# Optimization experiments

Measured on AMD Instinct MI355X. Metric: run time of the kernel, lower is better.

The kernel has to match this reference:

```python
import jax, jax.numpy as jnp
import numpy as np
from jax import lax

NUM_CLASSES = 80
CONF = 0.05
IOU_T = 0.5
K_PER_CLASS = 100   # max_detections_per_class
MAX_DET = 100       # max_detections
BOX_VAR = np.array([0.1, 0.1, 0.2, 0.2], dtype=np.float32)


def make_anchors(H, W):
    """AnchorBox.get_anchors: [x, y, w, h] anchors for strides 8..128."""
    ratios = [0.5, 1.0, 2.0]
    scales = [2.0 ** 0, 2.0 ** (1.0 / 3.0), 2.0 ** (2.0 / 3.0)]
    strides = [8, 16, 32, 64, 128]
    areas = [32.0 ** 2, 64.0 ** 2, 128.0 ** 2, 256.0 ** 2, 512.0 ** 2]
    out = []
    for stride, area in zip(strides, areas):
        fh = int(np.ceil(H / stride)); fw = int(np.ceil(W / stride))
        dims = []
        for r in ratios:
            ah = np.sqrt(area / r); aw = area / ah
            for s in scales:
                dims.append([aw * s, ah * s])
        dims = np.array(dims, dtype=np.float32)              # [9,2]
        rx = (np.arange(fw, dtype=np.float32) + 0.5) * stride
        ry = (np.arange(fh, dtype=np.float32) + 0.5) * stride
        cx, cy = np.meshgrid(rx, ry)                         # [fh,fw]
        centers = np.stack([cx, cy], axis=-1)                # [fh,fw,2]
        centers = np.tile(centers[:, :, None, :], (1, 1, 9, 1))
        d = np.tile(dims[None, None, :, :], (fh, fw, 1, 1))
        out.append(np.concatenate([centers, d], axis=-1).reshape(-1, 4))
    return np.concatenate(out, axis=0).astype(np.float32)   # [N,4]


def _iou_matrix(boxes):
    # boxes: [K,4] corner format (x1,y1,x2,y2)
    lt = jnp.maximum(boxes[:, None, :2], boxes[None, :, :2])
    rb = jnp.minimum(boxes[:, None, 2:], boxes[None, :, 2:])
    inter = jnp.prod(jnp.clip(rb - lt, 0.0), axis=-1)
    area = jnp.prod(boxes[:, 2:] - boxes[:, :2], axis=-1)
    union = area[:, None] + area[None, :] - inter
    return inter / jnp.maximum(union, 1e-8)


def _decode(predictions, anchors):
    box_pred = predictions[..., :4] * jnp.asarray(BOX_VAR)
    xy = box_pred[..., :2] * anchors[:, 2:] + anchors[:, :2]
    wh = jnp.exp(box_pred[..., 2:]) * anchors[:, 2:]
    boxes = jnp.concatenate([xy - wh / 2.0, xy + wh / 2.0], axis=-1)  # [B,N,4] corners
    cls = jax.nn.sigmoid(predictions[..., 4:])                        # [B,N,C]
    return boxes, cls


def _nms_image(boxes, cls_scores):
    # boxes [N,4], cls_scores [N,C]
    rng = jnp.arange(K_PER_CLASS)

    def per_class(scores):  # [N]
        top_s, idx = lax.top_k(scores, K_PER_CLASS)
        cb = boxes[idx]                                      # [K,4]
        iou = lax.stop_gradient(_iou_matrix(cb))
        keep0 = top_s > CONF
        def body(i, keep):
            sup = keep[i] & (iou[i] > IOU_T) & (rng > i)
            return keep & (~sup)
        keep = lax.fori_loop(0, K_PER_CLASS, body, keep0)
        return cb, jnp.where(keep, top_s, -1.0)

    cboxes, cscores = jax.vmap(per_class)(cls_scores.T)      # [C,K,4], [C,K]
    cids = jnp.broadcast_to(jnp.arange(NUM_CLASSES, dtype=jnp.float32)[:, None],
                            (NUM_CLASSES, K_PER_CLASS))
    flat_s = cscores.reshape(-1)
    flat_b = cboxes.reshape(-1, 4)
    flat_c = cids.reshape(-1)
    fs, fi = lax.top_k(flat_s, MAX_DET)
    fb = flat_b[fi]
    fc = flat_c[fi]
    mask = fs > 0.0
    valid = jnp.sum(mask).astype(jnp.int32)
    return (jnp.where(mask[:, None], fb, 0.0),
            jnp.where(mask, fs, 0.0),
            jnp.where(mask, fc, 0.0),
            valid)


def setup_inputs() -> dict:
    key = jax.random.key(0)
    k1, k2 = jax.random.split(key)
    images = jax.random.normal(k1, (8, 512, 512, 3), dtype=jnp.float32)
    predictions = jax.random.normal(k2, (8, 49104, 84), dtype=jnp.float32)
    return {"images": images, "predictions": predictions}


def reference(images, predictions):
    H, W = images.shape[1], images.shape[2]
    anchors = jnp.asarray(make_anchors(H, W))                # [49104,4]
    boxes, cls = _decode(predictions, anchors)
    nmsed_boxes, nmsed_scores, nmsed_classes, valid = jax.vmap(_nms_image)(boxes, cls)
    return nmsed_boxes, nmsed_scores, nmsed_classes, valid
```

## Files before the change

### kernel.cpp

```cpp
#include <hip/hip_runtime.h>
#include <math.h>
#include <stdint.h>

#define NANCH 49104
#define NCLS 80
#define KSEL 100
#define NFLAT (NCLS * KSEL)
#define PREDC 84
#define NB 8
#define ECAP 128
#define CAP 3072
#define BATF4 (NANCH * (PREDC / 4))
#define BPB 128
#define LCAP 32
#define FASTN 512
#define RMAX 8
#define CNTP 16
#define THRL 2.5f

struct DimsTable { float d[5][9][2]; };
struct KT { uint32_t key; int tie; };

__device__ __forceinline__ uint32_t f2key(float f) {
    uint32_t u = __float_as_uint(f);
    return u ^ (uint32_t((int32_t)u >> 31) | 0x80000000u);
}
__device__ __forceinline__ float key2f(uint32_t k) {
    uint32_t u = (k & 0x80000000u) ? (k ^ 0x80000000u) : ~k;
    return __uint_as_float(u);
}
__device__ __forceinline__ float sigm(float x) { return 1.0f / (1.0f + expf(-x)); }

__device__ __forceinline__ void decode_box(const float4 pv, int n,
                                           const DimsTable& dt, float box[4]) {
    int lev, base, fw, stride;
    if (n < 36864)      { lev = 0; base = 0;     fw = 64; stride = 8;   }
    else if (n < 46080) { lev = 1; base = 36864; fw = 32; stride = 16;  }
    else if (n < 48384) { lev = 2; base = 46080; fw = 16; stride = 32;  }
    else if (n < 48960) { lev = 3; base = 48384; fw = 8;  stride = 64;  }
    else                { lev = 4; base = 48960; fw = 4;  stride = 128; }
    int i = n - base;
    int k = i % 9;
    int cell = i / 9;
    int xq = cell % fw, yq = cell / fw;
    float cx = ((float)xq + 0.5f) * (float)stride;
    float cy = ((float)yq + 0.5f) * (float)stride;
    float aw = dt.d[lev][k][0];
    float ah = dt.d[lev][k][1];
    float tx = __fmul_rn(pv.x, 0.1f);
    float ty = __fmul_rn(pv.y, 0.1f);
    float tw = __fmul_rn(pv.z, 0.2f);
    float th = __fmul_rn(pv.w, 0.2f);
    float px = __fadd_rn(__fmul_rn(tx, aw), cx);
    float py = __fadd_rn(__fmul_rn(ty, ah), cy);
    float pw = __fmul_rn(expf(tw), aw);
    float ph = __fmul_rn(expf(th), ah);
    float hw = __fmul_rn(pw, 0.5f);
    float hh = __fmul_rn(ph, 0.5f);
    box[0] = __fsub_rn(px, hw);
    box[1] = __fsub_rn(py, hh);
    box[2] = __fadd_rn(px, hw);
    box[3] = __fadd_rn(py, hh);
}

struct alignas(16) SelSh {
    int hist[4][2048];
    int suffix[256];
    uint32_t candKey[KSEL];
    int candIdx[KSEL];
    uint32_t eIdx[ECAP];
    uint32_t sKey[KSEL];
    int sIdx[KSEL];
    int cntG, cntE, krem, newkrem, digit, flast, rmin;
    uint32_t prefix, thrKey;
};

template <typename G>
__device__ int block_select(G get, int N, int K, SelSh& sh) {
    const int tid = threadIdx.x;
    const int wid = tid >> 6;
    int Ksel = (N < K) ? N : K;
    if (Ksel <= 0) return 0;

    if (N <= K) {
        if (tid < N) { KT e = get(tid); sh.candKey[tid] = e.key; sh.candIdx[tid] = e.tie; }
        __syncthreads();
        if (tid < N) {
            uint32_t mk = sh.candKey[tid]; int mi = sh.candIdx[tid];
            int rank = 0;
            for (int j = 0; j < N; ++j) {
                uint32_t kj = sh.candKey[j]; int ij = sh.candIdx[j];
                rank += (kj > mk) || (kj == mk && ij < mi);
            }
            sh.sKey[rank] = mk; sh.sIdx[rank] = mi;
        }
        __syncthreads();
        return Ksel;
    }

    if (tid == 0) { sh.krem = K; sh.prefix = 0; }
    for (int pass = 0; pass < 3; ++pass) {
        const int bins   = (pass == 2) ? 1024 : 2048;
        const int dshift = (pass == 0) ? 21 : (pass == 1 ? 10 : 0);
        const int fshift = (pass == 1) ? 21 : 10;
        const int dmask  = bins - 1;
        const bool multi = (pass == 0);
        if (multi) { for (int j = tid; j < 4 * 2048; j += 256) ((int*)sh.hist)[j] = 0; }
        else       { for (int j = tid; j < bins; j += 256) sh.hist[0][j] = 0; }
        __syncthreads();
        const uint32_t pref = sh.prefix;
        for (int i = tid; i < N; i += 256) {
            uint32_t key = get(i).key;
            if (pass == 0) {
                atomicAdd(&sh.hist[wid][(key >> dshift) & dmask], 1);
            } else if ((key >> fshift) == pref) {
                atomicAdd(&sh.hist[0][(key >> dshift) & dmask], 1);
            }
        }
        __syncthreads();
        if (multi) {
            for (int j = tid; j < bins; j += 256)
                sh.hist[0][j] += sh.hist[1][j] + sh.hist[2][j] + sh.hist[3][j];
            __syncthreads();
        }
        const int cpb = bins / 256;
        const int base = tid * cpb;
        int lsum = 0;
        for (int j = 0; j < cpb; ++j) lsum += sh.hist[0][base + j];
        sh.suffix[tid] = lsum;
        __syncthreads();
        for (int off = 1; off < 256; off <<= 1) {
            int v = (tid + off < 256) ? sh.suffix[tid + off] : 0;
            __syncthreads();
            sh.suffix[tid] += v;
            __syncthreads();
        }
        {
            int cum = sh.suffix[tid] - lsum;
            const int krem = sh.krem;
            for (int j = cpb - 1; j >= 0; --j) {
                int cnt = sh.hist[0][base + j];
                if (cnt > 0 && cum < krem && cum + cnt >= krem) {
                    sh.digit = base + j;
                    sh.newkrem = krem - cum;
                }
                cum += cnt;
            }
        }
        __syncthreads();
        if (tid == 0) {
            sh.krem = sh.newkrem;
            if (pass == 0)      sh.prefix = (uint32_t)sh.digit;
            else if (pass == 1) sh.prefix = (sh.prefix << 11) | (uint32_t)sh.digit;
            else                sh.thrKey = (sh.prefix << 10) | (uint32_t)sh.digit;
        }
        __syncthreads();
    }

    if (tid == 0) { sh.cntG = 0; sh.cntE = 0; }
    __syncthreads();
    const uint32_t thr = sh.thrKey;
    for (int i = tid; i < N; i += 256) {
        KT e = get(i);
        if (e.key > thr) {
            int g = atomicAdd(&sh.cntG, 1);
            sh.candKey[g] = e.key; sh.candIdx[g] = e.tie;
        } else if (e.key == thr) {
            int idx = atomicAdd(&sh.cntE, 1);
            if (idx < ECAP) sh.eIdx[idx] = (uint32_t)e.tie;
        }
    }
    __syncthreads();
    const int need = sh.krem;
    const int nG = K - need;
    if (sh.cntE <= ECAP) {
        const int ce = sh.cntE;
        if (tid < ce) {
            uint32_t my = sh.eIdx[tid];
            int rank = 0;
            for (int j = 0; j < ce; ++j) rank += (sh.eIdx[j] < my);
            if (rank < need) { sh.candKey[nG + rank] = thr; sh.candIdx[nG + rank] = (int)my; }
        }
    } else {
        if (tid == 0) sh.flast = -1;
        __syncthreads();
        for (int t = 0; t < need; ++t) {
            if (tid == 0) sh.rmin = 0x7FFFFFFF;
            __syncthreads();
            const int fl = sh.flast;
            int lmin = 0x7FFFFFFF;
            for (int i = tid; i < N; i += 256) {
                KT e = get(i);
                if (e.key == thr && e.tie > fl) lmin = min(lmin, e.tie);
            }
            atomicMin(&sh.rmin, lmin);
            __syncthreads();
            if (tid == 0) { sh.candKey[nG + t] = thr; sh.candIdx[nG + t] = sh.rmin; sh.flast = sh.rmin; }
            __syncthreads();
        }
    }
    __syncthreads();
    if (tid < K) {
        uint32_t mk = sh.candKey[tid]; int mi = sh.candIdx[tid];
        int rank = 0;
        for (int j = 0; j < K; ++j) {
            uint32_t kj = sh.candKey[j]; int ij = sh.candIdx[j];
            rank += (kj > mk) || (kj == mk && ij < mi);
        }
        sh.sKey[rank] = mk; sh.sIdx[rank] = mi;
    }
    __syncthreads();
    return Ksel;
}

__global__ __launch_bounds__(256) void init_k(int* __restrict__ cnt) {
    for (int x = threadIdx.x; x < (NB * NCLS + NB) * CNTP; x += 256) cnt[x] = 0;
}

__device__ __forceinline__ void procf4(float4 p, int v, int b,
                                       int* lcnt, uint2 (*buck)[LCAP],
                                       int* cnt, uint2* cand) {
    uint32_t q = (uint32_t)v / 21u;
    uint32_t j = (uint32_t)v - q * 21u;
    if (j == 0u) return;
    bool c0 = p.x > THRL, c1 = p.y > THRL, c2 = p.z > THRL, c3 = p.w > THRL;
    if (!(c0 | c1 | c2 | c3)) return;
    uint32_t row = q - (uint32_t)b * (uint32_t)NANCH;
    int cbase = ((int)j - 1) * 4;
    float vv[4] = {p.x, p.y, p.z, p.w};
    bool pp[4] = {c0, c1, c2, c3};
#pragma unroll
    for (int k = 0; k < 4; ++k) {
        if (pp[k]) {
            int c = cbase + k;
            uint32_t key = f2key(sigm(vv[k]));
            int slot = atomicAdd(&lcnt[c], 1);
            if (slot < LCAP) {
                buck[c][slot] = make_uint2(key, row);
            } else {
                int bc = b * NCLS + c;
                int gs = atomicAdd(&cnt[bc * CNTP], 1);
                if (gs < CAP) cand[(size_t)bc * CAP + gs] = make_uint2(key, row);
            }
        }
    }
}

__global__ __launch_bounds__(256) void cand_scan(const float4* __restrict__ predv,
                                                 uint2* __restrict__ cand,
                                                 int* __restrict__ cnt) {
    __shared__ uint2 buck[NCLS][LCAP];
    __shared__ int lcnt[NCLS];
    __shared__ int gbase[NCLS];

    const int tid = threadIdx.x;
    const int b = blockIdx.x / BPB;
    const int part = blockIdx.x - b * BPB;
    const int CH = (BATF4 + BPB - 1) / BPB;

    for (int j = tid; j < NCLS; j += 256) lcnt[j] = 0;
    __syncthreads();

    int s = b * BATF4 + part * CH;
    int e = b * BATF4 + BATF4;
    if (s + CH < e) e = s + CH;

    int v = s + tid;
    for (; v + 7 * 256 < e; v += 8 * 256) {
        float4 a0 = predv[v];
        float4 a1 = predv[v + 1 * 256];
        float4 a2 = predv[v + 2 * 256];
        float4 a3 = predv[v + 3 * 256];
        float4 a4 = predv[v + 4 * 256];
        float4 a5 = predv[v + 5 * 256];
        float4 a6 = predv[v + 6 * 256];
        float4 a7 = predv[v + 7 * 256];
        procf4(a0, v,           b, lcnt, buck, cnt, cand);
        procf4(a1, v + 1 * 256, b, lcnt, buck, cnt, cand);
        procf4(a2, v + 2 * 256, b, lcnt, buck, cnt, cand);
        procf4(a3, v + 3 * 256, b, lcnt, buck, cnt, cand);
        procf4(a4, v + 4 * 256, b, lcnt, buck, cnt, cand);
        procf4(a5, v + 5 * 256, b, lcnt, buck, cnt, cand);
        procf4(a6, v + 6 * 256, b, lcnt, buck, cnt, cand);
        procf4(a7, v + 7 * 256, b, lcnt, buck, cnt, cand);
    }
    for (; v < e; v += 256)
        procf4(predv[v], v, b, lcnt, buck, cnt, cand);
    __syncthreads();

    if (tid < NCLS) {
        int lc = lcnt[tid];
        if (lc > LCAP) lc = LCAP;
        gbase[tid] = (lc > 0) ? atomicAdd(&cnt[(b * NCLS + tid) * CNTP], lc) : 0;
    }
    __syncthreads();

    for (int x = tid; x < NCLS * LCAP; x += 256) {
        int c = x >> 5;
        int k = x & (LCAP - 1);
        int lc = lcnt[c];
        if (lc > LCAP) lc = LCAP;
        if (k < lc) {
            int gs = gbase[c] + k;
            if (gs < CAP)
                cand[(size_t)(b * NCLS + c) * CAP + gs] = buck[c][k];
        }
    }
}

__global__ __launch_bounds__(256) void nms_sel(const float* __restrict__ pred,
                                               const uint2* __restrict__ cand,
                                               const int* __restrict__ cnt,
                                               float* __restrict__ cls_boxes,
                                               uint32_t* __restrict__ posKey,
                                               uint32_t* __restrict__ posFlat,
                                               int* __restrict__ posCnt,
                                               DimsTable dt) {
    __shared__ SelSh sh;
    __shared__ uint16_t prank[4][FASTN];
    __shared__ float sbox[KSEL][4];
    __shared__ float sarea[KSEL];
    __shared__ int sconf[KSEL];
    __shared__ uint32_t sup[KSEL][4];
    __shared__ uint32_t keepm[4];
    __shared__ int baseSh;
    const int c = blockIdx.x;
    const int b = blockIdx.y;
    const int tid = threadIdx.x;
    const int bc = b * NCLS + c;
    const int n = cnt[bc * CNTP];

    if (n >= KSEL && n <= FASTN) {
        unsigned long long* list64 = (unsigned long long*)sh.hist;
        const uint2* src = cand + (size_t)bc * CAP;
        for (int x = tid; x < n; x += 256) {
            uint2 p = src[x];
            list64[x] = ((unsigned long long)p.x << 32) |
                        (unsigned long long)(~p.y);
        }
        __syncthreads();
        const int wid = tid >> 6;
        const int lane = tid & 63;
        unsigned long long cl[RMAX];
        int pr[RMAX];
#pragma unroll
        for (int r = 0; r < RMAX; ++r) {
            int i = r * 64 + lane;
            cl[r] = (i < n) ? list64[i] : 0xFFFFFFFFFFFFFFFFull;
            pr[r] = 0;
        }
        const int js = (wid * n) >> 2;
        const int je = ((wid + 1) * n) >> 2;
        int j = js;
        for (; j + 3 < je; j += 4) {
            unsigned long long o0 = list64[j];
            unsigned long long o1 = list64[j + 1];
            unsigned long long o2 = list64[j + 2];
            unsigned long long o3 = list64[j + 3];
#pragma unroll
            for (int r = 0; r < RMAX; ++r)
                pr[r] += (o0 > cl[r]) + (o1 > cl[r]) + (o2 > cl[r]) + (o3 > cl[r]);
        }
        for (; j < je; ++j) {
            unsigned long long o = list64[j];
#pragma unroll
            for (int r = 0; r < RMAX; ++r) pr[r] += (o > cl[r]);
        }
#pragma unroll
        for (int r = 0; r < RMAX; ++r) {
            int i = r * 64 + lane;
            if (i < n) prank[wid][i] = (uint16_t)pr[r];
        }
        __syncthreads();
        for (int i = tid; i < n; i += 256) {
            int rank = (int)prank[0][i] + (int)prank[1][i]
                     + (int)prank[2][i] + (int)prank[3][i];
            if (rank < KSEL) {
                unsigned long long e = list64[i];
                sh.sKey[rank] = (uint32_t)(e >> 32);
                sh.sIdx[rank] = (int)(~(uint32_t)e);
            }
        }
        __syncthreads();
    } else {
        const float* src = pred + (size_t)b * NANCH * PREDC + 4 + c;
        auto g = [src](int i) { KT e; e.key = f2key(sigm(src[(size_t)i * PREDC])); e.tie = i; return e; };
        block_select(g, NANCH, KSEL, sh);
    }

    for (int x = tid; x < KSEL * 4; x += 256) ((uint32_t*)sup)[x] = 0;
    if (tid < KSEL) {
        int ni = sh.sIdx[tid];
        float4 pv = reinterpret_cast<const float4*>(pred)[((size_t)b * NANCH + ni) * (PREDC / 4)];
        float bx[4]; decode_box(pv, ni, dt, bx);
        sbox[tid][0] = bx[0]; sbox[tid][1] = bx[1];
        sbox[tid][2] = bx[2]; sbox[tid][3] = bx[3];
        sarea[tid] = __fmul_rn(__fsub_rn(bx[2], bx[0]), __fsub_rn(bx[3], bx[1]));
        sconf[tid] = (key2f(sh.sKey[tid]) > 0.05f) ? 1 : 0;
    }
    __syncthreads();

    for (int pidx = tid; pidx < KSEL * KSEL; pidx += 256) {
        int i = pidx / KSEL;
        int jj = pidx - i * KSEL;
        if (jj > i && sconf[i] && sconf[jj]) {
            float x1 = fmaxf(sbox[i][0], sbox[jj][0]);
            float y1 = fmaxf(sbox[i][1], sbox[jj][1]);
            float x2 = fminf(sbox[i][2], sbox[jj][2]);
            float y2 = fminf(sbox[i][3], sbox[jj][3]);
            float iw = fmaxf(__fsub_rn(x2, x1), 0.0f);
            float ih = fmaxf(__fsub_rn(y2, y1), 0.0f);
            float inter = __fmul_rn(iw, ih);
            float uni = __fsub_rn(__fadd_rn(sarea[i], sarea[jj]), inter);
            if (__fdiv_rn(inter, fmaxf(uni, 1e-8f)) > 0.5f)
                atomicOr(&sup[i][jj >> 5], 1u << (jj & 31));
        }
    }
    __syncthreads();

    if (tid == 0) {
        uint32_t k0 = 0, k1 = 0, k2 = 0, k3 = 0;
        for (int i = 0; i < KSEL; ++i)
            if (sconf[i]) { if (i < 32) k0 |= 1u << i; else if (i < 64) k1 |= 1u << (i - 32);
                            else if (i < 96) k2 |= 1u << (i - 64); else k3 |= 1u << (i - 96); }
        for (int i = 0; i < KSEL; ++i) {
            uint32_t w = (i < 32) ? k0 : (i < 64) ? k1 : (i < 96) ? k2 : k3;
            if ((w >> (i & 31)) & 1u) {
                k0 &= ~sup[i][0]; k1 &= ~sup[i][1]; k2 &= ~sup[i][2]; k3 &= ~sup[i][3];
            }
        }
        keepm[0] = k0; keepm[1] = k1; keepm[2] = k2; keepm[3] = k3;
        baseSh = atomicAdd(&posCnt[b * CNTP],
                           __popc(k0) + __popc(k1) + __popc(k2) + __popc(k3));
    }
    __syncthreads();

    if (tid < KSEL) {
        reinterpret_cast<float4*>(cls_boxes)[(size_t)b * NFLAT + c * KSEL + tid] =
            make_float4(sbox[tid][0], sbox[tid][1], sbox[tid][2], sbox[tid][3]);
        int w = tid >> 5, bit = tid & 31;
        if ((keepm[w] >> bit) & 1u) {
            int off = __popc(keepm[w] & ((bit == 0) ? 0u : ((1u << bit) - 1u)));
            for (int ww = 0; ww < w; ++ww) off += __popc(keepm[ww]);
            posKey[(size_t)b * NFLAT + baseSh + off] = sh.sKey[tid];
            posFlat[(size_t)b * NFLAT + baseSh + off] = (uint32_t)(c * KSEL + tid);
        }
    }
}

__global__ __launch_bounds__(256) void final_sel(const float* __restrict__ cls_boxes,
                                                 const uint32_t* __restrict__ posKey,
                                                 const uint32_t* __restrict__ posFlat,
                                                 const int* __restrict__ posCnt,
                                                 float* __restrict__ out) {
    __shared__ SelSh sh;
    const int b = blockIdx.x;
    const int tid = threadIdx.x;
    int m = posCnt[b * CNTP];
    if (m > NFLAT) m = NFLAT;
    const uint32_t* pk = posKey + (size_t)b * NFLAT;
    const uint32_t* pf = posFlat + (size_t)b * NFLAT;
    auto g = [pk, pf](int i) { KT e; e.key = pk[i]; e.tie = (int)pf[i]; return e; };
    int K = block_select(g, m, KSEL, sh);
    if (tid < KSEL) {
        float4 ob = make_float4(0.f, 0.f, 0.f, 0.f);
        float sv = 0.f, cv = 0.f;
        if (tid < K) {
            sv = key2f(sh.sKey[tid]);
            int flat = sh.sIdx[tid];
            ob = reinterpret_cast<const float4*>(cls_boxes)[(size_t)b * NFLAT + flat];
            cv = (float)(flat / KSEL);
        }
        reinterpret_cast<float4*>(out)[(size_t)b * KSEL + tid] = ob;
        out[NB * KSEL * 4 + b * KSEL + tid] = sv;
        out[NB * KSEL * 5 + b * KSEL + tid] = cv;
    }
    if (tid == 0) out[NB * KSEL * 6 + b] = (float)K;
}

extern "C" void kernel_launch(void* const* d_in, const int* in_sizes, int n_in,
                              void* d_out, int out_size, void* d_ws, size_t ws_size,
                              hipStream_t stream) {
    const float* pred = (const float*)d_in[1];
    float* out = (float*)d_out;

    DimsTable dt;
    const double areasd[5] = {1024.0, 4096.0, 16384.0, 65536.0, 262144.0};
    const double ratios[3] = {0.5, 1.0, 2.0};
    const double scales[3] = {1.0, pow(2.0, 1.0 / 3.0), pow(2.0, 2.0 / 3.0)};
    for (int l = 0; l < 5; ++l)
        for (int ri = 0; ri < 3; ++ri) {
            double ah = sqrt(areasd[l] / ratios[ri]);
            double aw = areasd[l] / ah;
            for (int si = 0; si < 3; ++si) {
                dt.d[l][ri * 3 + si][0] = (float)(aw * scales[si]);
                dt.d[l][ri * 3 + si][1] = (float)(ah * scales[si]);
            }
        }

    char* wsb = (char*)d_ws;
    int* cnt = (int*)wsb;
    int* posCnt = cnt + NB * NCLS * CNTP;
    uint2* cand = (uint2*)(wsb + 64 * 1024);
    float* cls_boxes = (float*)((char*)cand + (size_t)NB * NCLS * CAP * 8);
    uint32_t* posKey = (uint32_t*)(cls_boxes + (size_t)NB * NFLAT * 4);
    uint32_t* posFlat = posKey + (size_t)NB * NFLAT;

    init_k<<<1, 256, 0, stream>>>(cnt);

    cand_scan<<<NB * BPB, 256, 0, stream>>>(reinterpret_cast<const float4*>(pred),
                                            cand, cnt);

    dim3 gb(NCLS, NB);
    nms_sel<<<gb, 256, 0, stream>>>(pred, cand, cnt, cls_boxes, posKey, posFlat,
                                    posCnt, dt);

    final_sel<<<NB, 256, 0, stream>>>(cls_boxes, posKey, posFlat, posCnt, out);
}
```

Before: 126.4 us.

## Replace global atomic candidate append with per-block slots and prefix-sum compaction

Candidate collection moves from per-class global atomic counters into fixed per-block slots (PCAP each), plus a small overflow buffer. Consumers now compact these slots with a block prefix sum, and the per-class kept lists are also written to fixed slots and compacted in final_sel. BPB is doubled, nms_sel uses a single-copy histogram to cut shared memory, and the greedy NMS keep-mask loop becomes a wavefront ballot/shuffle. This is meant to remove global atomic contention and give deterministic ordering, at the cost of extra prefix scans and a serial compaction copy in final_sel.

```diff
diff --git a/kernel.cpp b/kernel.cpp
--- a/kernel.cpp
+++ b/kernel.cpp
@@ -9,17 +9,18 @@
 #define PREDC 84
 #define NB 8
 #define ECAP 128
-#define CAP 3072
 #define BATF4 (NANCH * (PREDC / 4))
-#define BPB 128
-#define LCAP 32
+#define BPB 256
+#define PCAP 16
+#define LCAP 16
+#define OCAP 64
 #define FASTN 512
 #define RMAX 8
-#define CNTP 16
 #define THRL 2.5f
 
 struct DimsTable { float d[5][9][2]; };
 struct KT { uint32_t key; int tie; };
+typedef unsigned long long u64;
 
 __device__ __forceinline__ uint32_t f2key(float f) {
     uint32_t u = __float_as_uint(f);
@@ -63,8 +64,9 @@
     box[3] = __fadd_rn(py, hh);
 }
 
-struct alignas(16) SelSh {
-    int hist[4][2048];
+template <int NC>
+struct alignas(16) SelShT {
+    int hist[NC][2048];
     int suffix[256];
     uint32_t candKey[KSEL];
     int candIdx[KSEL];
@@ -75,8 +77,8 @@
     uint32_t prefix, thrKey;
 };
 
-template <typename G>
-__device__ int block_select(G get, int N, int K, SelSh& sh) {
+template <int NC, typename G>
+__device__ int block_select(G get, int N, int K, SelShT<NC>& sh) {
     const int tid = threadIdx.x;
     const int wid = tid >> 6;
     int Ksel = (N < K) ? N : K;
@@ -104,23 +106,25 @@
         const int dshift = (pass == 0) ? 21 : (pass == 1 ? 10 : 0);
         const int fshift = (pass == 1) ? 21 : 10;
         const int dmask  = bins - 1;
-        const bool multi = (pass == 0);
-        if (multi) { for (int j = tid; j < 4 * 2048; j += 256) ((int*)sh.hist)[j] = 0; }
-        else       { for (int j = tid; j < bins; j += 256) sh.hist[0][j] = 0; }
+        if (pass == 0) { for (int j = tid; j < NC * 2048; j += 256) ((int*)sh.hist)[j] = 0; }
+        else           { for (int j = tid; j < bins; j += 256) sh.hist[0][j] = 0; }
         __syncthreads();
         const uint32_t pref = sh.prefix;
         for (int i = tid; i < N; i += 256) {
             uint32_t key = get(i).key;
             if (pass == 0) {
-                atomicAdd(&sh.hist[wid][(key >> dshift) & dmask], 1);
+                atomicAdd(&sh.hist[(NC > 1) ? wid : 0][(key >> dshift) & dmask], 1);
             } else if ((key >> fshift) == pref) {
                 atomicAdd(&sh.hist[0][(key >> dshift) & dmask], 1);
             }
         }
         __syncthreads();
-        if (multi) {
-            for (int j = tid; j < bins; j += 256)
-                sh.hist[0][j] += sh.hist[1][j] + sh.hist[2][j] + sh.hist[3][j];
+        if (NC > 1 && pass == 0) {
+            for (int j = tid; j < bins; j += 256) {
+                int s = sh.hist[0][j];
+                for (int cc = 1; cc < NC; ++cc) s += sh.hist[cc][j];
+                sh.hist[0][j] = s;
+            }
             __syncthreads();
         }
         const int cpb = bins / 256;
@@ -213,13 +217,13 @@
     return Ksel;
 }
 
-__global__ __launch_bounds__(256) void init_k(int* __restrict__ cnt) {
-    for (int x = threadIdx.x; x < (NB * NCLS + NB) * CNTP; x += 256) cnt[x] = 0;
+__global__ __launch_bounds__(256) void init_k(int* __restrict__ oflowCnt) {
+    for (int x = threadIdx.x; x < NB * NCLS; x += 256) oflowCnt[x] = 0;
 }
 
 __device__ __forceinline__ void procf4(float4 p, int v, int b,
                                        int* lcnt, uint2 (*buck)[LCAP],
-                                       int* cnt, uint2* cand) {
+                                       int* oflowCnt, uint2* oflow) {
     uint32_t q = (uint32_t)v / 21u;
     uint32_t j = (uint32_t)v - q * 21u;
     if (j == 0u) return;
@@ -239,19 +243,20 @@
                 buck[c][slot] = make_uint2(key, row);
             } else {
                 int bc = b * NCLS + c;
-                int gs = atomicAdd(&cnt[bc * CNTP], 1);
-                if (gs < CAP) cand[(size_t)bc * CAP + gs] = make_uint2(key, row);
+                int gs = atomicAdd(&oflowCnt[bc], 1);
+                if (gs < OCAP) oflow[(size_t)bc * OCAP + gs] = make_uint2(key, row);
             }
         }
     }
 }
 
 __global__ __launch_bounds__(256) void cand_scan(const float4* __restrict__ predv,
-                                                 uint2* __restrict__ cand,
-                                                 int* __restrict__ cnt) {
+                                                 uint2* __restrict__ cand2,
+                                                 int* __restrict__ cnt2,
+                                                 int* __restrict__ oflowCnt,
+                                                 uint2* __restrict__ oflow) {
     __shared__ uint2 buck[NCLS][LCAP];
     __shared__ int lcnt[NCLS];
-    __shared__ int gbase[NCLS];
 
     const int tid = threadIdx.x;
     const int b = blockIdx.x / BPB;
@@ -275,73 +280,85 @@
         float4 a5 = predv[v + 5 * 256];
         float4 a6 = predv[v + 6 * 256];
         float4 a7 = predv[v + 7 * 256];
-        procf4(a0, v,           b, lcnt, buck, cnt, cand);
-        procf4(a1, v + 1 * 256, b, lcnt, buck, cnt, cand);
-        procf4(a2, v + 2 * 256, b, lcnt, buck, cnt, cand);
-        procf4(a3, v + 3 * 256, b, lcnt, buck, cnt, cand);
-        procf4(a4, v + 4 * 256, b, lcnt, buck, cnt, cand);
-        procf4(a5, v + 5 * 256, b, lcnt, buck, cnt, cand);
-        procf4(a6, v + 6 * 256, b, lcnt, buck, cnt, cand);
-        procf4(a7, v + 7 * 256, b, lcnt, buck, cnt, cand);
+        procf4(a0, v,           b, lcnt, buck, oflowCnt, oflow);
+        procf4(a1, v + 1 * 256, b, lcnt, buck, oflowCnt, oflow);
+        procf4(a2, v + 2 * 256, b, lcnt, buck, oflowCnt, oflow);
+        procf4(a3, v + 3 * 256, b, lcnt, buck, oflowCnt, oflow);
+        procf4(a4, v + 4 * 256, b, lcnt, buck, oflowCnt, oflow);
+        procf4(a5, v + 5 * 256, b, lcnt, buck, oflowCnt, oflow);
+        procf4(a6, v + 6 * 256, b, lcnt, buck, oflowCnt, oflow);
+        procf4(a7, v + 7 * 256, b, lcnt, buck, oflowCnt, oflow);
     }
     for (; v < e; v += 256)
-        procf4(predv[v], v, b, lcnt, buck, cnt, cand);
+        procf4(predv[v], v, b, lcnt, buck, oflowCnt, oflow);
     __syncthreads();
 
     if (tid < NCLS) {
         int lc = lcnt[tid];
         if (lc > LCAP) lc = LCAP;
-        gbase[tid] = (lc > 0) ? atomicAdd(&cnt[(b * NCLS + tid) * CNTP], lc) : 0;
-    }
-    __syncthreads();
-
+        cnt2[((size_t)b * NCLS + tid) * BPB + part] = lc;
+    }
     for (int x = tid; x < NCLS * LCAP; x += 256) {
-        int c = x >> 5;
+        int c = x >> 4;
         int k = x & (LCAP - 1);
         int lc = lcnt[c];
         if (lc > LCAP) lc = LCAP;
-        if (k < lc) {
-            int gs = gbase[c] + k;
-            if (gs < CAP)
-                cand[(size_t)(b * NCLS + c) * CAP + gs] = buck[c][k];
-        }
+        if (k < lc)
+            cand2[(((size_t)b * NCLS + c) * BPB + part) * PCAP + k] = buck[c][k];
     }
 }
 
 __global__ __launch_bounds__(256) void nms_sel(const float* __restrict__ pred,
-                                               const uint2* __restrict__ cand,
-                                               const int* __restrict__ cnt,
+                                               const uint2* __restrict__ cand2,
+                                               const int* __restrict__ cnt2,
+                                               const int* __restrict__ oflowCnt,
+                                               const uint2* __restrict__ oflow,
                                                float* __restrict__ cls_boxes,
-                                               uint32_t* __restrict__ posKey,
-                                               uint32_t* __restrict__ posFlat,
-                                               int* __restrict__ posCnt,
+                                               uint32_t* __restrict__ posKeyC,
+                                               uint32_t* __restrict__ posFlatC,
+                                               int* __restrict__ posCntC,
                                                DimsTable dt) {
-    __shared__ SelSh sh;
+    __shared__ SelShT<1> sh;
     __shared__ uint16_t prank[4][FASTN];
     __shared__ float sbox[KSEL][4];
     __shared__ float sarea[KSEL];
     __shared__ int sconf[KSEL];
-    __shared__ uint32_t sup[KSEL][4];
+    __shared__ alignas(16) uint32_t sup[KSEL][4];
     __shared__ uint32_t keepm[4];
-    __shared__ int baseSh;
     const int c = blockIdx.x;
     const int b = blockIdx.y;
     const int tid = threadIdx.x;
     const int bc = b * NCLS + c;
-    const int n = cnt[bc * CNTP];
-
-    if (n >= KSEL && n <= FASTN) {
-        unsigned long long* list64 = (unsigned long long*)sh.hist;
-        const uint2* src = cand + (size_t)bc * CAP;
-        for (int x = tid; x < n; x += 256) {
-            uint2 p = src[x];
-            list64[x] = ((unsigned long long)p.x << 32) |
-                        (unsigned long long)(~p.y);
+
+    int myc = cnt2[(size_t)bc * BPB + tid];
+    sh.suffix[tid] = myc;
+    __syncthreads();
+    for (int off = 1; off < 256; off <<= 1) {
+        int v = (tid >= off) ? sh.suffix[tid - off] : 0;
+        __syncthreads();
+        sh.suffix[tid] += v;
+        __syncthreads();
+    }
+    const int excl = sh.suffix[tid] - myc;
+    const int n0 = sh.suffix[255];
+    const int of = oflowCnt[bc];
+    const int n = n0 + of;
+
+    if (n >= KSEL && n <= FASTN && of <= OCAP) {
+        u64* list64 = (u64*)sh.hist;
+        const uint2* sl = cand2 + ((size_t)bc * BPB + tid) * PCAP;
+        for (int k = 0; k < myc; ++k) {
+            uint2 p = sl[k];
+            list64[excl + k] = ((u64)p.x << 32) | (u64)(~p.y);
+        }
+        for (int x = tid; x < of; x += 256) {
+            uint2 p = oflow[(size_t)bc * OCAP + x];
+            list64[n0 + x] = ((u64)p.x << 32) | (u64)(~p.y);
         }
         __syncthreads();
         const int wid = tid >> 6;
         const int lane = tid & 63;
-        unsigned long long cl[RMAX];
+        u64 cl[RMAX];
         int pr[RMAX];
 #pragma unroll
         for (int r = 0; r < RMAX; ++r) {
@@ -353,16 +370,16 @@
         const int je = ((wid + 1) * n) >> 2;
         int j = js;
         for (; j + 3 < je; j += 4) {
-            unsigned long long o0 = list64[j];
-            unsigned long long o1 = list64[j + 1];
-            unsigned long long o2 = list64[j + 2];
-            unsigned long long o3 = list64[j + 3];
+            u64 o0 = list64[j];
+            u64 o1 = list64[j + 1];
+            u64 o2 = list64[j + 2];
+            u64 o3 = list64[j + 3];
 #pragma unroll
             for (int r = 0; r < RMAX; ++r)
                 pr[r] += (o0 > cl[r]) + (o1 > cl[r]) + (o2 > cl[r]) + (o3 > cl[r]);
         }
         for (; j < je; ++j) {
-            unsigned long long o = list64[j];
+            u64 o = list64[j];
 #pragma unroll
             for (int r = 0; r < RMAX; ++r) pr[r] += (o > cl[r]);
         }
@@ -376,7 +393,7 @@
             int rank = (int)prank[0][i] + (int)prank[1][i]
                      + (int)prank[2][i] + (int)prank[3][i];
             if (rank < KSEL) {
-                unsigned long long e = list64[i];
+                u64 e = list64[i];
                 sh.sKey[rank] = (uint32_t)(e >> 32);
                 sh.sIdx[rank] = (int)(~(uint32_t)e);
             }
@@ -385,7 +402,7 @@
     } else {
         const float* src = pred + (size_t)b * NANCH * PREDC + 4 + c;
         auto g = [src](int i) { KT e; e.key = f2key(sigm(src[(size_t)i * PREDC])); e.tie = i; return e; };
-        block_select(g, NANCH, KSEL, sh);
+        block_select<1>(g, NANCH, KSEL, sh);
     }
 
     for (int x = tid; x < KSEL * 4; x += 256) ((uint32_t*)sup)[x] = 0;
@@ -418,20 +435,38 @@
     }
     __syncthreads();
 
-    if (tid == 0) {
-        uint32_t k0 = 0, k1 = 0, k2 = 0, k3 = 0;
-        for (int i = 0; i < KSEL; ++i)
-            if (sconf[i]) { if (i < 32) k0 |= 1u << i; else if (i < 64) k1 |= 1u << (i - 32);
-                            else if (i < 96) k2 |= 1u << (i - 64); else k3 |= 1u << (i - 96); }
+    if (tid < 64) {
+        const int l = tid;
+        uint4 rowA = *reinterpret_cast<const uint4*>(sup[l]);
+        int confA = sconf[l];
+        uint4 rowB = make_uint4(0u, 0u, 0u, 0u);
+        int confB = 0;
+        if (l + 64 < KSEL) {
+            rowB = *reinterpret_cast<const uint4*>(sup[l + 64]);
+            confB = sconf[l + 64];
+        }
+        u64 mA = __ballot(confA != 0);
+        u64 mB = __ballot(confB != 0);
+        uint32_t k0 = (uint32_t)mA, k1 = (uint32_t)(mA >> 32);
+        uint32_t k2 = (uint32_t)mB, k3 = (uint32_t)(mB >> 32);
         for (int i = 0; i < KSEL; ++i) {
             uint32_t w = (i < 32) ? k0 : (i < 64) ? k1 : (i < 96) ? k2 : k3;
             if ((w >> (i & 31)) & 1u) {
-                k0 &= ~sup[i][0]; k1 &= ~sup[i][1]; k2 &= ~sup[i][2]; k3 &= ~sup[i][3];
-            }
-        }
-        keepm[0] = k0; keepm[1] = k1; keepm[2] = k2; keepm[3] = k3;
-        baseSh = atomicAdd(&posCnt[b * CNTP],
-                           __popc(k0) + __popc(k1) + __popc(k2) + __popc(k3));
+                uint32_t s0, s1, s2, s3;
+                if (i < 64) {
+                    s0 = __shfl(rowA.x, i); s1 = __shfl(rowA.y, i);
+                    s2 = __shfl(rowA.z, i); s3 = __shfl(rowA.w, i);
+                } else {
+                    s0 = __shfl(rowB.x, i - 64); s1 = __shfl(rowB.y, i - 64);
+                    s2 = __shfl(rowB.z, i - 64); s3 = __shfl(rowB.w, i - 64);
+                }
+                k0 &= ~s0; k1 &= ~s1; k2 &= ~s2; k3 &= ~s3;
+            }
+        }
+        if (l == 0) {
+            keepm[0] = k0; keepm[1] = k1; keepm[2] = k2; keepm[3] = k3;
+            posCntC[bc] = __popc(k0) + __popc(k1) + __popc(k2) + __popc(k3);
+        }
     }
     __syncthreads();
 
@@ -442,26 +477,47 @@
         if ((keepm[w] >> bit) & 1u) {
             int off = __popc(keepm[w] & ((bit == 0) ? 0u : ((1u << bit) - 1u)));
             for (int ww = 0; ww < w; ++ww) off += __popc(keepm[ww]);
-            posKey[(size_t)b * NFLAT + baseSh + off] = sh.sKey[tid];
-            posFlat[(size_t)b * NFLAT + baseSh + off] = (uint32_t)(c * KSEL + tid);
+            posKeyC[(size_t)bc * KSEL + off] = sh.sKey[tid];
+            posFlatC[(size_t)bc * KSEL + off] = (uint32_t)(c * KSEL + tid);
         }
     }
 }
 
 __global__ __launch_bounds__(256) void final_sel(const float* __restrict__ cls_boxes,
-                                                 const uint32_t* __restrict__ posKey,
-                                                 const uint32_t* __restrict__ posFlat,
-                                                 const int* __restrict__ posCnt,
+                                                 const uint32_t* __restrict__ posKeyC,
+                                                 const uint32_t* __restrict__ posFlatC,
+                                                 const int* __restrict__ posCntC,
+                                                 uint32_t* __restrict__ compKey,
+                                                 uint32_t* __restrict__ compFlat,
                                                  float* __restrict__ out) {
-    __shared__ SelSh sh;
+    __shared__ SelShT<4> sh;
     const int b = blockIdx.x;
     const int tid = threadIdx.x;
-    int m = posCnt[b * CNTP];
-    if (m > NFLAT) m = NFLAT;
-    const uint32_t* pk = posKey + (size_t)b * NFLAT;
-    const uint32_t* pf = posFlat + (size_t)b * NFLAT;
+
+    int myc = (tid < NCLS) ? posCntC[b * NCLS + tid] : 0;
+    sh.suffix[tid] = myc;
+    __syncthreads();
+    for (int off = 1; off < 256; off <<= 1) {
+        int v = (tid >= off) ? sh.suffix[tid - off] : 0;
+        __syncthreads();
+        sh.suffix[tid] += v;
+        __syncthreads();
+    }
+    const int excl = sh.suffix[tid] - myc;
+    const int m = sh.suffix[255];
+    if (tid < NCLS) {
+        const size_t sbase = (size_t)(b * NCLS + tid) * KSEL;
+        for (int k = 0; k < myc; ++k) {
+            compKey[(size_t)b * NFLAT + excl + k] = posKeyC[sbase + k];
+            compFlat[(size_t)b * NFLAT + excl + k] = posFlatC[sbase + k];
+        }
+    }
+    __syncthreads();
+
+    const uint32_t* pk = compKey + (size_t)b * NFLAT;
+    const uint32_t* pf = compFlat + (size_t)b * NFLAT;
     auto g = [pk, pf](int i) { KT e; e.key = pk[i]; e.tie = (int)pf[i]; return e; };
-    int K = block_select(g, m, KSEL, sh);
+    int K = block_select<4>(g, m, KSEL, sh);
     if (tid < KSEL) {
         float4 ob = make_float4(0.f, 0.f, 0.f, 0.f);
         float sv = 0.f, cv = 0.f;
@@ -499,21 +555,26 @@
         }
 
     char* wsb = (char*)d_ws;
-    int* cnt = (int*)wsb;
-    int* posCnt = cnt + NB * NCLS * CNTP;
-    uint2* cand = (uint2*)(wsb + 64 * 1024);
-    float* cls_boxes = (float*)((char*)cand + (size_t)NB * NCLS * CAP * 8);
-    uint32_t* posKey = (uint32_t*)(cls_boxes + (size_t)NB * NFLAT * 4);
-    uint32_t* posFlat = posKey + (size_t)NB * NFLAT;
-
-    init_k<<<1, 256, 0, stream>>>(cnt);
+    int* oflowCnt = (int*)wsb;
+    int* posCntC  = oflowCnt + NB * NCLS;
+    uint2* oflow  = (uint2*)(wsb + 8192);
+    uint2* cand2  = oflow + (size_t)NB * NCLS * OCAP;
+    int* cnt2     = (int*)(cand2 + (size_t)NB * NCLS * BPB * PCAP);
+    float* cls_boxes = (float*)(cnt2 + (size_t)NB * NCLS * BPB);
+    uint32_t* posKeyC  = (uint32_t*)(cls_boxes + (size_t)NB * NFLAT * 4);
+    uint32_t* posFlatC = posKeyC + (size_t)NB * NFLAT;
+    uint32_t* compKey  = posFlatC + (size_t)NB * NFLAT;
+    uint32_t* compFlat = compKey + (size_t)NB * NFLAT;
+
+    init_k<<<1, 256, 0, stream>>>(oflowCnt);
 
     cand_scan<<<NB * BPB, 256, 0, stream>>>(reinterpret_cast<const float4*>(pred),
-                                            cand, cnt);
+                                            cand2, cnt2, oflowCnt, oflow);
 
     dim3 gb(NCLS, NB);
-    nms_sel<<<gb, 256, 0, stream>>>(pred, cand, cnt, cls_boxes, posKey, posFlat,
-                                    posCnt, dt);
-
-    final_sel<<<NB, 256, 0, stream>>>(cls_boxes, posKey, posFlat, posCnt, out);
-}
+    nms_sel<<<gb, 256, 0, stream>>>(pred, cand2, cnt2, oflowCnt, oflow,
+                                    cls_boxes, posKeyC, posFlatC, posCntC, dt);
+
+    final_sel<<<NB, 256, 0, stream>>>(cls_boxes, posKeyC, posFlatC, posCntC,
+                                      compKey, compFlat, out);
+}
```

After: 136.1 us. +7.7%, slower.
